# Optimization experiments

Measured on AMD Instinct MI355X. Metric: run time of the kernel, lower is better.

## Reference

```python
import jax, jax.numpy as jnp
import numpy as np
import math

B, T, D, H, DM = 2, 2048, 1024, 16, 256
DK = D // H

def setup_inputs() -> dict:
    key = jax.random.key(0)
    ks = jax.random.split(key, 13)
    s = 0.02
    return {
        "Hx": jax.random.normal(ks[0], (B, D, T, 1), jnp.float32),
        "Hf": jax.random.normal(ks[1], (B, T, D), jnp.float32),
        "Gm": jax.random.normal(ks[2], (B, T, DM), jnp.float32),
        "Wg": jax.random.normal(ks[3], (T, DM), jnp.float32) * s,
        "bg": jax.random.normal(ks[4], (T,), jnp.float32) * s,
        "Wq": jax.random.normal(ks[5], (D, 2 * D), jnp.float32) * s,
        "bq": jax.random.normal(ks[6], (D,), jnp.float32) * s,
        "Wk": jax.random.normal(ks[7], (D, 2 * D), jnp.float32) * s,
        "bk": jax.random.normal(ks[8], (D,), jnp.float32) * s,
        "Wv": jax.random.normal(ks[9], (D, D), jnp.float32) * s,
        "bv": jax.random.normal(ks[10], (D,), jnp.float32) * s,
        "Wo": jax.random.normal(ks[11], (D, D), jnp.float32) * s,
        "bo": jax.random.normal(ks[12], (D,), jnp.float32) * s,
    }

def reference(Hx, Hf, Gm, Wg, bg, Wq, bq, Wk, bk, Wv, bv, Wo, bo):
    # Hx: (B, D, T, 1) -> (B, T, D)
    hx = jnp.transpose(Hx[..., 0], (0, 2, 1))
    h_cat = jnp.concatenate([hx, Hf], axis=-1)          # (B, T, 2D)
    Q = h_cat @ Wq.T + bq                               # (B, T, D)
    K = h_cat @ Wk.T + bk
    V = hx @ Wv.T + bv
    # split heads: (B, H, T, DK)
    Q = Q.reshape(B, T, H, DK).transpose(0, 2, 1, 3)
    K = K.reshape(B, T, H, DK).transpose(0, 2, 1, 3)
    V = V.reshape(B, T, H, DK).transpose(0, 2, 1, 3)
    scores = jnp.einsum('bhqd,bhkd->bhqk', Q, K) / math.sqrt(DK)
    bias = Gm @ Wg.T + bg                                # (B, T, T)
    scores = scores + bias[:, None, :, :]
    attn = jax.nn.softmax(scores, axis=-1)
    out = jnp.einsum('bhqk,bhkd->bhqd', attn, V)
    out = out.transpose(0, 2, 1, 3).reshape(B, T, D)
    return out @ Wo.T + bo
```

## Files before the change

### kernel.cpp

```cpp
#include <hip/hip_runtime.h>
#include <hip/hip_bf16.h>

using bf16 = __hip_bfloat16;
typedef __attribute__((ext_vector_type(8))) __bf16 bf16x8;
typedef __attribute__((ext_vector_type(4))) float f32x4;

#define GLB_AS(p) ((const __attribute__((address_space(1))) unsigned int*)(p))
#define LDS_AS(p) ((__attribute__((address_space(3))) unsigned int*)(p))

__device__ __forceinline__ void async_copy16(const void* g, void* l) {
  __builtin_amdgcn_global_load_lds(GLB_AS(g), LDS_AS(l), 16, 0, 0);
}

__device__ __forceinline__ f32x4 mfma16x16x32(bf16x8 a, bf16x8 b, f32x4 c) {
  return __builtin_amdgcn_mfma_f32_16x16x32_bf16(a, b, c, 0, 0, 0);
}

__device__ __forceinline__ float bfu2f(unsigned short u) {
  union { unsigned int i; float f; } x;
  x.i = (unsigned int)u << 16;
  return x.f;
}

#define LOG2E 1.44269504f

__global__ __launch_bounds__(256) void pack_hx(const float* __restrict__ Hx,
                                               bf16* __restrict__ hcat) {
  __shared__ float tile[64][65];
  const int t0 = blockIdx.x * 64, d0 = blockIdx.y * 64, b = blockIdx.z;
  const int c = threadIdx.x & 63, r0 = threadIdx.x >> 6;
#pragma unroll
  for (int i = 0; i < 16; ++i) {
    const int rd = r0 + i * 4;
    tile[rd][c] = Hx[((size_t)(b * 1024 + d0 + rd)) * 2048 + t0 + c];
  }
  __syncthreads();
#pragma unroll
  for (int i = 0; i < 16; ++i) {
    const int ct = r0 + i * 4;
    hcat[((size_t)(b * 2048 + t0 + ct)) * 2048 + d0 + c] =
        __float2bfloat16(tile[c][ct]);
  }
}

__global__ __launch_bounds__(256) void pack_all(
    const float* __restrict__ Hf, const float* __restrict__ Wq,
    const float* __restrict__ Wk, const float* __restrict__ Wv,
    const float* __restrict__ Wo, const float* __restrict__ Wg,
    const float* __restrict__ Gm, const float* __restrict__ bq,
    const float* __restrict__ bk, const float* __restrict__ bv,
    bf16* __restrict__ hcat, bf16* __restrict__ Wqkvb, bf16* __restrict__ Wob,
    bf16* __restrict__ Wgb, bf16* __restrict__ Gmb,
    float* __restrict__ qkvbias) {
  const int gid = blockIdx.x * 256 + threadIdx.x;
  const float* src = nullptr;
  bf16* dst = nullptr;
  int lg = 0, ldo = 0, off = 0, idx = 0;
  bool zero = false;
  if (gid < 1048576) { idx = gid; src = Hf; dst = hcat; lg = 8; ldo = 2048; off = 1024; }
  else if (gid < 1572864) { idx = gid - 1048576; src = Wq; dst = Wqkvb; lg = 9; ldo = 2048; }
  else if (gid < 2097152) { idx = gid - 1572864; src = Wk; dst = Wqkvb + (size_t)1024 * 2048; lg = 9; ldo = 2048; }
  else if (gid < 2359296) { idx = gid - 2097152; src = Wv; dst = Wqkvb + (size_t)2048 * 2048; lg = 8; ldo = 2048; }
  else if (gid < 2621440) { idx = gid - 2359296; zero = true; dst = Wqkvb + (size_t)2048 * 2048 + 1024; lg = 8; ldo = 2048; }
  else if (gid < 2883584) { idx = gid - 2621440; src = Wo; dst = Wob; lg = 8; ldo = 1024; }
  else if (gid < 3014656) { idx = gid - 2883584; src = Wg; dst = Wgb; lg = 6; ldo = 256; }
  else if (gid < 3276800) { idx = gid - 3014656; src = Gm; dst = Gmb; lg = 6; ldo = 256; }
  else if (gid < 3277056) { const int i = gid - 3276800; ((float4*)qkvbias)[i] = ((const float4*)bq)[i]; return; }
  else if (gid < 3277312) { const int i = gid - 3277056; ((float4*)(qkvbias + 1024))[i] = ((const float4*)bk)[i]; return; }
  else { const int i = gid - 3277312; ((float4*)(qkvbias + 2048))[i] = ((const float4*)bv)[i]; return; }
  const int row = idx >> lg, c = idx & ((1 << lg) - 1);
  bf16* o = dst + (size_t)row * ldo + off + c * 4;
  __align__(8) bf16 tmp[4];
  if (zero) {
    tmp[0] = tmp[1] = tmp[2] = tmp[3] = __float2bfloat16(0.f);
  } else {
    const float4 v = ((const float4*)src)[(size_t)idx];
    tmp[0] = __float2bfloat16(v.x); tmp[1] = __float2bfloat16(v.y);
    tmp[2] = __float2bfloat16(v.z); tmp[3] = __float2bfloat16(v.w);
  }
  *(ushort4*)o = *(const ushort4*)tmp;
}

__global__ __launch_bounds__(256) void gemm_qkv_bias(
    const bf16* __restrict__ hcat, const bf16* __restrict__ Wqkv,
    const float* __restrict__ qkvbias, const bf16* __restrict__ Gmb,
    const bf16* __restrict__ Wgb, const float* __restrict__ bg,
    bf16* __restrict__ QKb, bf16* __restrict__ Vt, bf16* __restrict__ biasS) {
  __shared__ __align__(16) bf16 As[2][128 * 64];
  __shared__ __align__(16) bf16 Bs[2][128 * 64];
  const int lin = blockIdx.x;
  const int xcd = lin & 7;
  const int kk = lin >> 3;
  const bool isqkv = kk < 96;
  int m_idx, n0;
  if (isqkv) {
    m_idx = kk / 3;
    n0 = (xcd * 3 + (kk - m_idx * 3)) * 128;
  } else {
    const int k2 = kk - 96;
    m_idx = k2 >> 1;
    n0 = (xcd * 2 + (k2 & 1)) * 128;
  }
  const int m0 = m_idx * 128;
  const bf16* A = isqkv ? hcat : Gmb;
  const bf16* W = isqkv ? Wqkv : Wgb;
  const float* biasv = isqkv ? qkvbias : bg;
  const int Kd = isqkv ? 2048 : 256;
  const int tid = threadIdx.x, lane = tid & 63, w = tid >> 6;
  const int wm = (w >> 1) * 64, wn = (w & 1) * 64;
  const int fr = lane & 15;
  const int ck = lane >> 4;

  f32x4 acc[4][4];
  const f32x4 fzero = {0.f, 0.f, 0.f, 0.f};
#pragma unroll
  for (int i = 0; i < 4; ++i)
#pragma unroll
    for (int j = 0; j < 4; ++j) acc[i][j] = fzero;

  auto stage = [&](int it, int buf) {
    const int k0 = it * 64;
#pragma unroll
    for (int is = 0; is < 4; ++is) {
      const int off = is * 4096 + w * 1024;
      const int row = (off >> 7) + (lane >> 3);
      const int sch = ((lane & 7) ^ (row & 7)) * 8;
      async_copy16(A + (size_t)(m0 + row) * Kd + k0 + sch,
                   (char*)As[buf] + off);
      async_copy16(W + (size_t)(n0 + row) * Kd + k0 + sch,
                   (char*)Bs[buf] + off);
    }
  };

  const int nit = Kd >> 6;
  stage(0, 0);
  __syncthreads();
  for (int it = 0; it < nit; ++it) {
    const int cur = it & 1;
    if (it + 1 < nit) stage(it + 1, cur ^ 1);
#pragma unroll
    for (int ks = 0; ks < 2; ++ks) {
      bf16x8 af[4], bfr[4];
#pragma unroll
      for (int i = 0; i < 4; ++i) {
        const int swk = (((ks * 4 + ck) ^ (fr & 7))) * 8;
        af[i] = *(const bf16x8*)(As[cur] + (wm + i * 16 + fr) * 64 + swk);
        bfr[i] = *(const bf16x8*)(Bs[cur] + (wn + i * 16 + fr) * 64 + swk);
      }
#pragma unroll
      for (int i = 0; i < 4; ++i)
#pragma unroll
        for (int j = 0; j < 4; ++j)
          acc[i][j] = mfma16x16x32(af[i], bfr[j], acc[i][j]);
    }
    __syncthreads();
  }
  const int erow = (lane >> 4) * 4;
  const int ecol = lane & 15;

  if (!isqkv) {
#pragma unroll
    for (int i = 0; i < 4; ++i) {
      const int gm0 = m0 + wm + i * 16 + erow;
#pragma unroll
      for (int j = 0; j < 4; ++j) {
        const int gn = n0 + wn + j * 16 + ecol;
        const float bv = biasv[gn];
#pragma unroll
        for (int r = 0; r < 4; ++r)
          biasS[(size_t)(gm0 + r) * 2048 + gn] =
              __float2bfloat16((acc[i][j][r] + bv) * LOG2E);
      }
    }
  } else if (n0 < 2048) {
    const float sc = (n0 < 1024) ? 0.125f * LOG2E : 1.0f;
#pragma unroll
    for (int i = 0; i < 4; ++i) {
      const int gm0 = m0 + wm + i * 16 + erow;
#pragma unroll
      for (int j = 0; j < 4; ++j) {
        const int gn = n0 + wn + j * 16 + ecol;
        const float bv = biasv[gn];
#pragma unroll
        for (int r = 0; r < 4; ++r)
          QKb[(size_t)(gm0 + r) * 2048 + gn] =
              __float2bfloat16((acc[i][j][r] + bv) * sc);
      }
    }
  } else {
#pragma unroll
    for (int i = 0; i < 4; ++i) {
      const int gm0 = m0 + wm + i * 16 + erow;
      const int bb = gm0 >> 11;
      const int t = gm0 & 2047;
#pragma unroll
      for (int j = 0; j < 4; ++j) {
        const int gn = n0 + wn + j * 16 + ecol;
        const float bv = biasv[gn];
        const int d = gn - 2048;
        __align__(8) bf16 tmp[4];
#pragma unroll
        for (int r = 0; r < 4; ++r)
          tmp[r] = __float2bfloat16(acc[i][j][r] + bv);
        *(ushort4*)(Vt + ((size_t)(bb * 1024 + d)) * 2048 + t) =
            *(const ushort4*)tmp;
      }
    }
  }
}

__global__ __launch_bounds__(256) void gemm_out(const bf16* __restrict__ A,
                                                const bf16* __restrict__ W,
                                                const float* __restrict__ biasv,
                                                float* __restrict__ C) {
  __shared__ __align__(16) bf16 As[2][128 * 64];
  __shared__ __align__(16) bf16 Bs[2][64 * 64];
  const int lin = blockIdx.x;
  const int xcd = lin & 7;
  const int kk = lin >> 3;
  const int m0 = (kk >> 1) * 128;
  const int n0 = (xcd * 2 + (kk & 1)) * 64;
  const int tid = threadIdx.x, lane = tid & 63, w = tid >> 6;
  const int wm = (w >> 1) * 64, wn = (w & 1) * 32;
  const int fr = lane & 15;
  const int ck = lane >> 4;

  f32x4 acc[4][2];
  const f32x4 fzero = {0.f, 0.f, 0.f, 0.f};
#pragma unroll
  for (int i = 0; i < 4; ++i)
#pragma unroll
    for (int j = 0; j < 2; ++j) acc[i][j] = fzero;

  auto stage = [&](int it, int buf) {
    const int k0 = it * 64;
#pragma unroll
    for (int is = 0; is < 4; ++is) {
      const int off = is * 4096 + w * 1024;
      const int row = (off >> 7) + (lane >> 3);
      const int sch = ((lane & 7) ^ (row & 7)) * 8;
      async_copy16(A + (size_t)(m0 + row) * 1024 + k0 + sch,
                   (char*)As[buf] + off);
      if (is < 2)
        async_copy16(W + (size_t)(n0 + row) * 1024 + k0 + sch,
                     (char*)Bs[buf] + off);
    }
  };

  stage(0, 0);
  __syncthreads();
  for (int it = 0; it < 16; ++it) {
    const int cur = it & 1;
    if (it + 1 < 16) stage(it + 1, cur ^ 1);
#pragma unroll
    for (int ks = 0; ks < 2; ++ks) {
      bf16x8 af[4], bfr[2];
      const int swk0 = (((ks * 4 + ck) ^ (fr & 7))) * 8;
#pragma unroll
      for (int i = 0; i < 4; ++i)
        af[i] = *(const bf16x8*)(As[cur] + (wm + i * 16 + fr) * 64 + swk0);
#pragma unroll
      for (int j = 0; j < 2; ++j)
        bfr[j] = *(const bf16x8*)(Bs[cur] + (wn + j * 16 + fr) * 64 + swk0);
#pragma unroll
      for (int i = 0; i < 4; ++i)
#pragma unroll
        for (int j = 0; j < 2; ++j)
          acc[i][j] = mfma16x16x32(af[i], bfr[j], acc[i][j]);
    }
    __syncthreads();
  }
  const int erow = (lane >> 4) * 4;
  const int ecol = lane & 15;
#pragma unroll
  for (int i = 0; i < 4; ++i) {
    const int gm0 = m0 + wm + i * 16 + erow;
#pragma unroll
    for (int j = 0; j < 2; ++j) {
      const int gn = n0 + wn + j * 16 + ecol;
      const float bv = biasv[gn];
#pragma unroll
      for (int r = 0; r < 4; ++r)
        C[(size_t)(gm0 + r) * 1024 + gn] = acc[i][j][r] + bv;
    }
  }
}

__global__ __launch_bounds__(256) void flash_attn(
    const bf16* __restrict__ Qm, const bf16* __restrict__ Km,
    const bf16* __restrict__ Vtm, const bf16* __restrict__ biasS,
    float* __restrict__ Op0, float* __restrict__ Op1,
    float* __restrict__ lpart) {
  __shared__ __align__(16) bf16 Ks[64 * 64];
  __shared__ __align__(16) bf16 Vs[64 * 64];
  __shared__ __align__(16) bf16 Ps[4 * 32 * 72];
  const int lin = blockIdx.x;
  const int xcd = lin & 7;
  const int kk = lin >> 3;
  const int cl = kk & 3;
  const int r2 = kk >> 2;
  const int half = r2 & 1;
  const int q0 = (r2 >> 1) * 128;
  const int combo = xcd * 4 + cl;
  const int h = combo & 15;
  const int b = combo >> 4;
  const int tid = threadIdx.x, lane = tid & 63, w = tid >> 6;
  const int ql = lane & 15, qk = lane >> 4;
  const int T = 2048, D = 1024;
  const int sw0 = (qk ^ (ql & 7)) * 8;
  const int sw1 = ((qk + 4) ^ (ql & 7)) * 8;

  bf16x8 qf[2][2];
#pragma unroll
  for (int qt = 0; qt < 2; ++qt)
#pragma unroll
    for (int ks = 0; ks < 2; ++ks)
      qf[qt][ks] = *(const bf16x8*)(
          Qm + (size_t)(b * T + q0 + w * 32 + qt * 16 + ql) * 2048 + h * 64 +
          ks * 32 + qk * 8);

  f32x4 acc[4][2];
  const f32x4 fzero = {0.f, 0.f, 0.f, 0.f};
#pragma unroll
  for (int dt = 0; dt < 4; ++dt)
#pragma unroll
    for (int qt = 0; qt < 2; ++qt) acc[dt][qt] = fzero;
  float lp[2] = {0.f, 0.f};

  const bf16* kbase = Km + (size_t)(b * T) * 2048 + h * 64;
  const bf16* vbase = Vtm + (size_t)(b * D + h * 64) * 2048;
  const bf16* bb0 = biasS + (size_t)(b * T + q0 + w * 32 + ql) * 2048 + qk * 4;
  bf16* pb = Ps + w * 2304;

  for (int j = 0; j < 16; ++j) {
    const int jj = half * 16 + j;
    __syncthreads();
#pragma unroll
    for (int is = 0; is < 2; ++is) {
      const int off = is * 4096 + w * 1024;
      const int row = (off >> 7) + (lane >> 3);
      const int sch = ((lane & 7) ^ (row & 7)) * 8;
      async_copy16(kbase + (size_t)(jj * 64 + row) * 2048 + sch,
                   (char*)Ks + off);
      async_copy16(vbase + (size_t)row * 2048 + jj * 64 + sch, (char*)Vs + off);
    }
    ushort4 bq[2][4];
#pragma unroll
    for (int qt = 0; qt < 2; ++qt)
#pragma unroll
      for (int jt = 0; jt < 4; ++jt)
        bq[qt][jt] = *(const ushort4*)(bb0 + (size_t)qt * 16 * 2048 + jj * 64 +
                                       jt * 16);
    __syncthreads();
#pragma unroll
    for (int jt = 0; jt < 4; ++jt) {
      const bf16x8 kf0 = *(const bf16x8*)(Ks + (jt * 16 + ql) * 64 + sw0);
      const bf16x8 kf1 = *(const bf16x8*)(Ks + (jt * 16 + ql) * 64 + sw1);
#pragma unroll
      for (int qt = 0; qt < 2; ++qt) {
        f32x4 c;
        c[0] = bfu2f(bq[qt][jt].x); c[1] = bfu2f(bq[qt][jt].y);
        c[2] = bfu2f(bq[qt][jt].z); c[3] = bfu2f(bq[qt][jt].w);
        c = mfma16x16x32(kf0, qf[qt][0], c);
        c = mfma16x16x32(kf1, qf[qt][1], c);
        __align__(8) bf16 t4[4];
#pragma unroll
        for (int r = 0; r < 4; ++r) {
          const float pv = __builtin_amdgcn_exp2f(c[r]);
          lp[qt] += pv;
          t4[r] = __float2bfloat16(pv);
        }
        *(ushort4*)(pb + (qt * 16 + ql) * 72 + jt * 16 + qk * 4) =
            *(const ushort4*)t4;
      }
    }
#pragma unroll
    for (int ks = 0; ks < 2; ++ks) {
      const bf16x8 pf0 = *(const bf16x8*)(pb + ql * 72 + ks * 32 + qk * 8);
      const bf16x8 pf1 =
          *(const bf16x8*)(pb + (16 + ql) * 72 + ks * 32 + qk * 8);
      const int sw = ks ? sw1 : sw0;
#pragma unroll
      for (int dt = 0; dt < 4; ++dt) {
        const bf16x8 vf = *(const bf16x8*)(Vs + (dt * 16 + ql) * 64 + sw);
        acc[dt][0] = mfma16x16x32(pf0, vf, acc[dt][0]);
        acc[dt][1] = mfma16x16x32(pf1, vf, acc[dt][1]);
      }
    }
  }
#pragma unroll
  for (int qt = 0; qt < 2; ++qt) {
    lp[qt] += __shfl_xor(lp[qt], 16);
    lp[qt] += __shfl_xor(lp[qt], 32);
  }
  if (qk == 0) {
#pragma unroll
    for (int qt = 0; qt < 2; ++qt)
      lpart[half * 65536 + (b * 16 + h) * 2048 + q0 + w * 32 + qt * 16 + ql] =
          lp[qt];
  }
  float* Op = half ? Op1 : Op0;
#pragma unroll
  for (int qt = 0; qt < 2; ++qt)
#pragma unroll
    for (int r = 0; r < 4; ++r) {
      const size_t orow = (size_t)(b * T + q0 + w * 32 + qt * 16 + qk * 4 + r);
#pragma unroll
      for (int dt = 0; dt < 4; ++dt)
        Op[orow * 1024 + h * 64 + dt * 16 + ql] = acc[dt][qt][r];
    }
}

__global__ __launch_bounds__(256) void combine(const float* __restrict__ O0,
                                               const float* __restrict__ O1,
                                               const float* __restrict__ lpart,
                                               bf16* __restrict__ AOut) {
  const int idx = blockIdx.x * 256 + threadIdx.x;
  const int row = idx >> 8;
  const int col = (idx & 255) * 4;
  const int b = row >> 11, q = row & 2047, h = col >> 6;
  const int li = (b * 16 + h) * 2048 + q;
  const float inv = __builtin_amdgcn_rcpf(lpart[li] + lpart[65536 + li]);
  const float4 a = *(const float4*)(O0 + (size_t)row * 1024 + col);
  const float4 c = *(const float4*)(O1 + (size_t)row * 1024 + col);
  __align__(8) bf16 t[4] = {
      __float2bfloat16((a.x + c.x) * inv), __float2bfloat16((a.y + c.y) * inv),
      __float2bfloat16((a.z + c.z) * inv), __float2bfloat16((a.w + c.w) * inv)};
  *(ushort4*)(AOut + (size_t)row * 1024 + col) = *(const ushort4*)t;
}

extern "C" void kernel_launch(void* const* d_in, const int* in_sizes, int n_in,
                              void* d_out, int out_size, void* d_ws,
                              size_t ws_size, hipStream_t stream) {
  (void)in_sizes; (void)n_in; (void)out_size; (void)ws_size;
  const float* Hx = (const float*)d_in[0];
  const float* Hf = (const float*)d_in[1];
  const float* Gm = (const float*)d_in[2];
  const float* Wg = (const float*)d_in[3];
  const float* bg = (const float*)d_in[4];
  const float* Wq = (const float*)d_in[5];
  const float* bq = (const float*)d_in[6];
  const float* Wk = (const float*)d_in[7];
  const float* bk = (const float*)d_in[8];
  const float* Wv = (const float*)d_in[9];
  const float* bv = (const float*)d_in[10];
  const float* Wo = (const float*)d_in[11];
  const float* bo = (const float*)d_in[12];
  float* out = (float*)d_out;

  char* p = (char*)d_ws;
  bf16* hcat = (bf16*)p;   p += (size_t)4096 * 2048 * 2;
  bf16* QKb = (bf16*)p;    p += (size_t)4096 * 2048 * 2;
  bf16* Vtb = (bf16*)p;    p += (size_t)4096 * 1024 * 2;
  bf16* biasS = (bf16*)p;  p += (size_t)4096 * 2048 * 2;
  bf16* AOut = (bf16*)p;   p += (size_t)4096 * 1024 * 2;
  bf16* Wqkvb = (bf16*)p;  p += (size_t)3072 * 2048 * 2;
  bf16* Wob = (bf16*)p;    p += (size_t)1024 * 1024 * 2;
  bf16* Wgb = (bf16*)p;    p += (size_t)2048 * 256 * 2;
  bf16* Gmb = (bf16*)p;    p += (size_t)4096 * 256 * 2;
  float* qkvbias = (float*)p; p += (size_t)3072 * 4;
  float* Op1 = (float*)p;  p += (size_t)4096 * 1024 * 4;
  float* lpart = (float*)p; p += (size_t)2 * 65536 * 4;
  float* Op0 = (float*)hcat;

  pack_hx<<<dim3(32, 16, 2), 256, 0, stream>>>(Hx, hcat);
  pack_all<<<dim3(12803), 256, 0, stream>>>(Hf, Wq, Wk, Wv, Wo, Wg, Gm, bq, bk,
                                            bv, hcat, Wqkvb, Wob, Wgb, Gmb,
                                            qkvbias);
  gemm_qkv_bias<<<dim3(1280), 256, 0, stream>>>(hcat, Wqkvb, qkvbias, Gmb,
                                                Wgb, bg, QKb, Vtb, biasS);
  flash_attn<<<dim3(1024), 256, 0, stream>>>(QKb, QKb + 1024, Vtb, biasS,
                                             Op0, Op1, lpart);
  combine<<<dim3(4096), 256, 0, stream>>>(Op0, Op1, lpart, AOut);
  gemm_out<<<dim3(512), 256, 0, stream>>>(AOut, Wob, bo, out);
}
```

Measured before the change: 306.3 us.

## Keep softmax probabilities in registers, feeding PV MFMA via 16x16x16 layout

Removes the LDS staging buffer for the probability tile in flash attention. The S=K·Q^T accumulator layout is reused directly as a B operand of 16x16x16 bf16 MFMAs against V fragments read with a matching swizzle. The output accumulators are transposed, so the final store changes to vectorized float4 writes per row. The cost is twice as many (half-K) MFMA issues and narrower V LDS reads.

```diff
diff --git a/kernel.cpp b/kernel.cpp
--- a/kernel.cpp
+++ b/kernel.cpp
@@ -4,6 +4,7 @@
 using bf16 = __hip_bfloat16;
 typedef __attribute__((ext_vector_type(8))) __bf16 bf16x8;
 typedef __attribute__((ext_vector_type(4))) float f32x4;
+typedef __attribute__((ext_vector_type(4))) short short4v;
 
 #define GLB_AS(p) ((const __attribute__((address_space(1))) unsigned int*)(p))
 #define LDS_AS(p) ((__attribute__((address_space(3))) unsigned int*)(p))
@@ -14,6 +15,10 @@
 
 __device__ __forceinline__ f32x4 mfma16x16x32(bf16x8 a, bf16x8 b, f32x4 c) {
   return __builtin_amdgcn_mfma_f32_16x16x32_bf16(a, b, c, 0, 0, 0);
+}
+
+__device__ __forceinline__ f32x4 mfma16x16x16(short4v a, short4v b, f32x4 c) {
+  return __builtin_amdgcn_mfma_f32_16x16x16bf16_1k(a, b, c, 0, 0, 0);
 }
 
 __device__ __forceinline__ float bfu2f(unsigned short u) {
@@ -293,7 +298,6 @@
     float* __restrict__ lpart) {
   __shared__ __align__(16) bf16 Ks[64 * 64];
   __shared__ __align__(16) bf16 Vs[64 * 64];
-  __shared__ __align__(16) bf16 Ps[4 * 32 * 72];
   const int lin = blockIdx.x;
   const int xcd = lin & 7;
   const int kk = lin >> 3;
@@ -330,7 +334,6 @@
   const bf16* kbase = Km + (size_t)(b * T) * 2048 + h * 64;
   const bf16* vbase = Vtm + (size_t)(b * D + h * 64) * 2048;
   const bf16* bb0 = biasS + (size_t)(b * T + q0 + w * 32 + ql) * 2048 + qk * 4;
-  bf16* pb = Ps + w * 2304;
 
   for (int j = 0; j < 16; ++j) {
     const int jj = half * 16 + j;
@@ -356,6 +359,7 @@
     for (int jt = 0; jt < 4; ++jt) {
       const bf16x8 kf0 = *(const bf16x8*)(Ks + (jt * 16 + ql) * 64 + sw0);
       const bf16x8 kf1 = *(const bf16x8*)(Ks + (jt * 16 + ql) * 64 + sw1);
+      short4v pfr[2];
 #pragma unroll
       for (int qt = 0; qt < 2; ++qt) {
         f32x4 c;
@@ -370,21 +374,14 @@
           lp[qt] += pv;
           t4[r] = __float2bfloat16(pv);
         }
-        *(ushort4*)(pb + (qt * 16 + ql) * 72 + jt * 16 + qk * 4) =
-            *(const ushort4*)t4;
-      }
-    }
-#pragma unroll
-    for (int ks = 0; ks < 2; ++ks) {
-      const bf16x8 pf0 = *(const bf16x8*)(pb + ql * 72 + ks * 32 + qk * 8);
-      const bf16x8 pf1 =
-          *(const bf16x8*)(pb + (16 + ql) * 72 + ks * 32 + qk * 8);
-      const int sw = ks ? sw1 : sw0;
+        pfr[qt] = *(const short4v*)t4;
+      }
 #pragma unroll
       for (int dt = 0; dt < 4; ++dt) {
-        const bf16x8 vf = *(const bf16x8*)(Vs + (dt * 16 + ql) * 64 + sw);
-        acc[dt][0] = mfma16x16x32(pf0, vf, acc[dt][0]);
-        acc[dt][1] = mfma16x16x32(pf1, vf, acc[dt][1]);
+        const int slot = ((jt * 2 + (qk >> 1)) ^ (ql & 7)) * 8 + (qk & 1) * 4;
+        const short4v vf = *(const short4v*)(Vs + (dt * 16 + ql) * 64 + slot);
+        acc[dt][0] = mfma16x16x16(vf, pfr[0], acc[dt][0]);
+        acc[dt][1] = mfma16x16x16(vf, pfr[1], acc[dt][1]);
       }
     }
   }
@@ -401,14 +398,16 @@
   }
   float* Op = half ? Op1 : Op0;
 #pragma unroll
-  for (int qt = 0; qt < 2; ++qt)
-#pragma unroll
-    for (int r = 0; r < 4; ++r) {
-      const size_t orow = (size_t)(b * T + q0 + w * 32 + qt * 16 + qk * 4 + r);
-#pragma unroll
-      for (int dt = 0; dt < 4; ++dt)
-        Op[orow * 1024 + h * 64 + dt * 16 + ql] = acc[dt][qt][r];
-    }
+  for (int qt = 0; qt < 2; ++qt) {
+    const size_t orow = (size_t)(b * T + q0 + w * 32 + qt * 16 + ql);
+#pragma unroll
+    for (int dt = 0; dt < 4; ++dt) {
+      float4 v;
+      v.x = acc[dt][qt][0]; v.y = acc[dt][qt][1];
+      v.z = acc[dt][qt][2]; v.w = acc[dt][qt][3];
+      *(float4*)(Op + orow * 1024 + h * 64 + dt * 16 + qk * 4) = v;
+    }
+  }
 }
 
 __global__ __launch_bounds__(256) void combine(const float* __restrict__ O0,
```

Result: slower. 321.9 us (+5.1%).

## Process two heads per flash-attention block to reuse bias tile loads

Applied to the files above, without the earlier changes.

Each flash_attn block now handles a pair of heads instead of one, loading K/V tiles for both heads into doubled LDS buffers while reading the shared attention bias tile once per key tile. This halves global bias traffic, which is shared across heads, and halves the grid to 512 blocks. In exchange it doubles LDS use and accumulator registers per block, which may reduce occupancy, and the smaller grid may underfill the GPU.

```diff
diff --git a/kernel.cpp b/kernel.cpp
--- a/kernel.cpp
+++ b/kernel.cpp
@@ -291,44 +291,48 @@
     const bf16* __restrict__ Vtm, const bf16* __restrict__ biasS,
     float* __restrict__ Op0, float* __restrict__ Op1,
     float* __restrict__ lpart) {
-  __shared__ __align__(16) bf16 Ks[64 * 64];
-  __shared__ __align__(16) bf16 Vs[64 * 64];
+  __shared__ __align__(16) bf16 Ks[2][64 * 64];
+  __shared__ __align__(16) bf16 Vs[2][64 * 64];
   __shared__ __align__(16) bf16 Ps[4 * 32 * 72];
   const int lin = blockIdx.x;
   const int xcd = lin & 7;
   const int kk = lin >> 3;
-  const int cl = kk & 3;
-  const int r2 = kk >> 2;
+  const int cl = kk & 1;
+  const int r2 = kk >> 1;
   const int half = r2 & 1;
   const int q0 = (r2 >> 1) * 128;
-  const int combo = xcd * 4 + cl;
-  const int h = combo & 15;
-  const int b = combo >> 4;
+  const int combo = xcd * 2 + cl;
+  const int hp = combo & 7;
+  const int b = combo >> 3;
   const int tid = threadIdx.x, lane = tid & 63, w = tid >> 6;
   const int ql = lane & 15, qk = lane >> 4;
   const int T = 2048, D = 1024;
   const int sw0 = (qk ^ (ql & 7)) * 8;
   const int sw1 = ((qk + 4) ^ (ql & 7)) * 8;
 
-  bf16x8 qf[2][2];
-#pragma unroll
-  for (int qt = 0; qt < 2; ++qt)
-#pragma unroll
-    for (int ks = 0; ks < 2; ++ks)
-      qf[qt][ks] = *(const bf16x8*)(
-          Qm + (size_t)(b * T + q0 + w * 32 + qt * 16 + ql) * 2048 + h * 64 +
-          ks * 32 + qk * 8);
-
-  f32x4 acc[4][2];
+  bf16x8 qf[2][2][2];
+#pragma unroll
+  for (int hh = 0; hh < 2; ++hh)
+#pragma unroll
+    for (int qt = 0; qt < 2; ++qt)
+#pragma unroll
+      for (int ks = 0; ks < 2; ++ks)
+        qf[hh][qt][ks] = *(const bf16x8*)(
+            Qm + (size_t)(b * T + q0 + w * 32 + qt * 16 + ql) * 2048 +
+            (hp * 2 + hh) * 64 + ks * 32 + qk * 8);
+
+  f32x4 acc[2][4][2];
   const f32x4 fzero = {0.f, 0.f, 0.f, 0.f};
 #pragma unroll
-  for (int dt = 0; dt < 4; ++dt)
-#pragma unroll
-    for (int qt = 0; qt < 2; ++qt) acc[dt][qt] = fzero;
-  float lp[2] = {0.f, 0.f};
-
-  const bf16* kbase = Km + (size_t)(b * T) * 2048 + h * 64;
-  const bf16* vbase = Vtm + (size_t)(b * D + h * 64) * 2048;
+  for (int hh = 0; hh < 2; ++hh)
+#pragma unroll
+    for (int dt = 0; dt < 4; ++dt)
+#pragma unroll
+      for (int qt = 0; qt < 2; ++qt) acc[hh][dt][qt] = fzero;
+  float lp[2][2] = {{0.f, 0.f}, {0.f, 0.f}};
+
+  const bf16* kbase0 = Km + (size_t)(b * T) * 2048 + (hp * 2) * 64;
+  const bf16* vbase0 = Vtm + (size_t)(b * D + hp * 2 * 64) * 2048;
   const bf16* bb0 = biasS + (size_t)(b * T + q0 + w * 32 + ql) * 2048 + qk * 4;
   bf16* pb = Ps + w * 2304;
 
@@ -336,14 +340,17 @@
     const int jj = half * 16 + j;
     __syncthreads();
 #pragma unroll
-    for (int is = 0; is < 2; ++is) {
-      const int off = is * 4096 + w * 1024;
-      const int row = (off >> 7) + (lane >> 3);
-      const int sch = ((lane & 7) ^ (row & 7)) * 8;
-      async_copy16(kbase + (size_t)(jj * 64 + row) * 2048 + sch,
-                   (char*)Ks + off);
-      async_copy16(vbase + (size_t)row * 2048 + jj * 64 + sch, (char*)Vs + off);
-    }
+    for (int hh = 0; hh < 2; ++hh)
+#pragma unroll
+      for (int is = 0; is < 2; ++is) {
+        const int off = is * 4096 + w * 1024;
+        const int row = (off >> 7) + (lane >> 3);
+        const int sch = ((lane & 7) ^ (row & 7)) * 8;
+        async_copy16(kbase0 + (size_t)(jj * 64 + row) * 2048 + hh * 64 + sch,
+                     (char*)Ks[hh] + off);
+        async_copy16(vbase0 + (size_t)(hh * 64 + row) * 2048 + jj * 64 + sch,
+                     (char*)Vs[hh] + off);
+      }
     ushort4 bq[2][4];
 #pragma unroll
     for (int qt = 0; qt < 2; ++qt)
@@ -353,62 +360,75 @@
                                        jt * 16);
     __syncthreads();
 #pragma unroll
-    for (int jt = 0; jt < 4; ++jt) {
-      const bf16x8 kf0 = *(const bf16x8*)(Ks + (jt * 16 + ql) * 64 + sw0);
-      const bf16x8 kf1 = *(const bf16x8*)(Ks + (jt * 16 + ql) * 64 + sw1);
-#pragma unroll
-      for (int qt = 0; qt < 2; ++qt) {
-        f32x4 c;
-        c[0] = bfu2f(bq[qt][jt].x); c[1] = bfu2f(bq[qt][jt].y);
-        c[2] = bfu2f(bq[qt][jt].z); c[3] = bfu2f(bq[qt][jt].w);
-        c = mfma16x16x32(kf0, qf[qt][0], c);
-        c = mfma16x16x32(kf1, qf[qt][1], c);
-        __align__(8) bf16 t4[4];
-#pragma unroll
-        for (int r = 0; r < 4; ++r) {
-          const float pv = __builtin_amdgcn_exp2f(c[r]);
-          lp[qt] += pv;
-          t4[r] = __float2bfloat16(pv);
+    for (int hh = 0; hh < 2; ++hh) {
+      const bf16* ksp = Ks[hh];
+      const bf16* vsp = Vs[hh];
+#pragma unroll
+      for (int jt = 0; jt < 4; ++jt) {
+        const bf16x8 kf0 = *(const bf16x8*)(ksp + (jt * 16 + ql) * 64 + sw0);
+        const bf16x8 kf1 = *(const bf16x8*)(ksp + (jt * 16 + ql) * 64 + sw1);
+#pragma unroll
+        for (int qt = 0; qt < 2; ++qt) {
+          f32x4 c;
+          c[0] = bfu2f(bq[qt][jt].x); c[1] = bfu2f(bq[qt][jt].y);
+          c[2] = bfu2f(bq[qt][jt].z); c[3] = bfu2f(bq[qt][jt].w);
+          c = mfma16x16x32(kf0, qf[hh][qt][0], c);
+          c = mfma16x16x32(kf1, qf[hh][qt][1], c);
+          __align__(8) bf16 t4[4];
+#pragma unroll
+          for (int r = 0; r < 4; ++r) {
+            const float pv = __builtin_amdgcn_exp2f(c[r]);
+            lp[hh][qt] += pv;
+            t4[r] = __float2bfloat16(pv);
+          }
+          *(ushort4*)(pb + (qt * 16 + ql) * 72 + jt * 16 + qk * 4) =
+              *(const ushort4*)t4;
         }
-        *(ushort4*)(pb + (qt * 16 + ql) * 72 + jt * 16 + qk * 4) =
-            *(const ushort4*)t4;
-      }
-    }
-#pragma unroll
-    for (int ks = 0; ks < 2; ++ks) {
-      const bf16x8 pf0 = *(const bf16x8*)(pb + ql * 72 + ks * 32 + qk * 8);
-      const bf16x8 pf1 =
-          *(const bf16x8*)(pb + (16 + ql) * 72 + ks * 32 + qk * 8);
-      const int sw = ks ? sw1 : sw0;
-#pragma unroll
-      for (int dt = 0; dt < 4; ++dt) {
-        const bf16x8 vf = *(const bf16x8*)(Vs + (dt * 16 + ql) * 64 + sw);
-        acc[dt][0] = mfma16x16x32(pf0, vf, acc[dt][0]);
-        acc[dt][1] = mfma16x16x32(pf1, vf, acc[dt][1]);
-      }
-    }
-  }
-#pragma unroll
-  for (int qt = 0; qt < 2; ++qt) {
-    lp[qt] += __shfl_xor(lp[qt], 16);
-    lp[qt] += __shfl_xor(lp[qt], 32);
-  }
+      }
+#pragma unroll
+      for (int ks = 0; ks < 2; ++ks) {
+        const bf16x8 pf0 = *(const bf16x8*)(pb + ql * 72 + ks * 32 + qk * 8);
+        const bf16x8 pf1 =
+            *(const bf16x8*)(pb + (16 + ql) * 72 + ks * 32 + qk * 8);
+        const int sw = ks ? sw1 : sw0;
+#pragma unroll
+        for (int dt = 0; dt < 4; ++dt) {
+          const bf16x8 vf = *(const bf16x8*)(vsp + (dt * 16 + ql) * 64 + sw);
+          acc[hh][dt][0] = mfma16x16x32(pf0, vf, acc[hh][dt][0]);
+          acc[hh][dt][1] = mfma16x16x32(pf1, vf, acc[hh][dt][1]);
+        }
+      }
+    }
+  }
+#pragma unroll
+  for (int hh = 0; hh < 2; ++hh)
+#pragma unroll
+    for (int qt = 0; qt < 2; ++qt) {
+      lp[hh][qt] += __shfl_xor(lp[hh][qt], 16);
+      lp[hh][qt] += __shfl_xor(lp[hh][qt], 32);
+    }
   if (qk == 0) {
 #pragma unroll
+    for (int hh = 0; hh < 2; ++hh)
+#pragma unroll
+      for (int qt = 0; qt < 2; ++qt)
+        lpart[half * 65536 + (b * 16 + hp * 2 + hh) * 2048 + q0 + w * 32 +
+              qt * 16 + ql] = lp[hh][qt];
+  }
+  float* Op = half ? Op1 : Op0;
+#pragma unroll
+  for (int hh = 0; hh < 2; ++hh)
+#pragma unroll
     for (int qt = 0; qt < 2; ++qt)
-      lpart[half * 65536 + (b * 16 + h) * 2048 + q0 + w * 32 + qt * 16 + ql] =
-          lp[qt];
-  }
-  float* Op = half ? Op1 : Op0;
-#pragma unroll
-  for (int qt = 0; qt < 2; ++qt)
-#pragma unroll
-    for (int r = 0; r < 4; ++r) {
-      const size_t orow = (size_t)(b * T + q0 + w * 32 + qt * 16 + qk * 4 + r);
-#pragma unroll
-      for (int dt = 0; dt < 4; ++dt)
-        Op[orow * 1024 + h * 64 + dt * 16 + ql] = acc[dt][qt][r];
-    }
+#pragma unroll
+      for (int r = 0; r < 4; ++r) {
+        const size_t orow =
+            (size_t)(b * T + q0 + w * 32 + qt * 16 + qk * 4 + r);
+#pragma unroll
+        for (int dt = 0; dt < 4; ++dt)
+          Op[orow * 1024 + (hp * 2 + hh) * 64 + dt * 16 + ql] =
+              acc[hh][dt][qt][r];
+      }
 }
 
 __global__ __launch_bounds__(256) void combine(const float* __restrict__ O0,
@@ -469,8 +489,8 @@
                                             qkvbias);
   gemm_qkv_bias<<<dim3(1280), 256, 0, stream>>>(hcat, Wqkvb, qkvbias, Gmb,
                                                 Wgb, bg, QKb, Vtb, biasS);
-  flash_attn<<<dim3(1024), 256, 0, stream>>>(QKb, QKb + 1024, Vtb, biasS,
-                                             Op0, Op1, lpart);
+  flash_attn<<<dim3(512), 256, 0, stream>>>(QKb, QKb + 1024, Vtb, biasS,
+                                            Op0, Op1, lpart);
   combine<<<dim3(4096), 256, 0, stream>>>(Op0, Op1, lpart, AOut);
   gemm_out<<<dim3(512), 256, 0, stream>>>(AOut, Wob, bo, out);
 }
```

Result: faster. 292.5 us (-4.5%).
